# Kernel tuning notes

Measured on AMD Instinct MI355X. Metric: run time of the kernel, lower is better.

The kernel has to match this reference:

```python
import jax, jax.numpy as jnp
import numpy as np
from jax.scipy.special import logsumexp

B, S, K = 512, 2048, 17

def setup_inputs() -> dict:
    key = jax.random.key(0)
    k_em, k_lab, k_len, k_st, k_en, k_tr = jax.random.split(key, 6)
    emissions = jax.random.normal(k_em, (B, S, K), dtype=jnp.float32)
    labels = jax.random.randint(k_lab, (B, S), 0, K, dtype=jnp.int64).astype(jnp.int32)
    # ragged valid-prefix mask; torchcrf requires mask[:, 0] to be all True
    lengths = jax.random.randint(k_len, (B,), 1, S + 1)
    attention_mask = (jnp.arange(S)[None, :] < lengths[:, None]).astype(jnp.int32)
    # CRF params (torchcrf inits uniform(-0.1, 0.1))
    start_transitions = jax.random.uniform(k_st, (K,), minval=-0.1, maxval=0.1, dtype=jnp.float32)
    end_transitions = jax.random.uniform(k_en, (K,), minval=-0.1, maxval=0.1, dtype=jnp.float32)
    transitions = jax.random.uniform(k_tr, (K, K), minval=-0.1, maxval=0.1, dtype=jnp.float32)
    return {
        "emissions": emissions,
        "start_transitions": start_transitions,
        "end_transitions": end_transitions,
        "transitions": transitions,
        "labels": labels,
        "attention_mask": attention_mask,
    }


def _crf_neg_log_likelihood(emissions, start_transitions, end_transitions, transitions,
                            labels, mask_bool):
    # emissions: [B,S,K], labels: [B,S] int, mask_bool: [B,S] bool (mask[:,0] all True)
    mask_f = mask_bool.astype(emissions.dtype)
    b_idx = jnp.arange(emissions.shape[0])

    # ---- numerator: score of the gold path ----
    first_tags = labels[:, 0]                                  # [B]
    num = start_transitions[first_tags] + emissions[b_idx, 0, first_tags]
    prev_tags = labels[:, :-1]                                 # [B,S-1]
    cur_tags = labels[:, 1:]                                   # [B,S-1]
    emit_t = jnp.take_along_axis(emissions[:, 1:, :], cur_tags[..., None], axis=-1)[..., 0]
    step_scores = transitions[prev_tags, cur_tags] + emit_t    # [B,S-1]
    num = num + jnp.sum(step_scores * mask_f[:, 1:], axis=1)
    seq_ends = jnp.sum(mask_bool, axis=1).astype(jnp.int32) - 1  # [B]
    last_tags = jnp.take_along_axis(labels, seq_ends[:, None], axis=1)[:, 0]
    num = num + end_transitions[last_tags]

    # ---- denominator: log partition via forward algorithm (lax.scan over time) ----
    alpha0 = start_transitions[None, :] + emissions[:, 0, :]   # [B,K]

    def step(alpha, xs):
        emit, m = xs                                           # emit [B,K], m [B] bool
        # alpha[b, i] + transitions[i, j] + emit[b, j] -> logsumexp over i
        nxt = logsumexp(alpha[:, :, None] + transitions[None, :, :] + emit[:, None, :], axis=1)
        alpha = jnp.where(m[:, None], nxt, alpha)
        return alpha, None

    em_seq = jnp.swapaxes(emissions[:, 1:, :], 0, 1)           # [S-1,B,K]
    m_seq = jnp.swapaxes(mask_bool[:, 1:], 0, 1)               # [S-1,B]
    alpha, _ = jax.lax.scan(step, alpha0, (em_seq, m_seq))
    log_z = logsumexp(alpha + end_transitions[None, :], axis=1)  # [B]

    llh = num - log_z
    return -jnp.mean(llh)  # torchcrf reduction='mean', loss = -crf(...)


def reference(emissions, start_transitions, end_transitions, transitions, labels, attention_mask):
    mask_bool = attention_mask.astype(bool) & (labels >= 0)
    labels_c = jnp.where(labels == -100, 0, labels)
    loss = _crf_neg_log_likelihood(emissions, start_transitions, end_transitions,
                                   transitions, labels_c, mask_bool)
    return loss, emissions
```

## Files before the change

### kernel.cpp

```cpp
#include <hip/hip_runtime.h>
#include <cstddef>

#define NB 512
#define NS 2048
#define NK 17
#define CL 8
#define NW 4
#define HT 1024
#define SP 8
#define NLT (HT + SP)
#define CHUNKD 37
#define ROWD 9
#define LDS_DW ((NLT / 4) * CHUNKD)
#define SLABF (HT * NK)

typedef __fp16 h2 __attribute__((ext_vector_type(2)));
typedef float  f4 __attribute__((ext_vector_type(4)));
union UH { unsigned int u; h2 h; };

__global__ void prep_k(const float* __restrict__ trans, const int* __restrict__ attn,
                       unsigned int* __restrict__ Mg, int* __restrict__ lens) {
    __shared__ int red[4];
    const int tid = threadIdx.x;
    if (blockIdx.x == 0) {
        if (tid < 9 * NK) {
            int kk = tid / NK, n = tid % NK;
            float lo = __expf(trans[(2 * kk) * NK + n]);
            float hi = (kk < 8) ? __expf(trans[(2 * kk + 1) * NK + n]) : 0.f;
            UH u; u.h = __builtin_amdgcn_cvt_pkrtz(lo, hi);
            Mg[tid] = u.u;
        }
        return;
    }
    const int b = blockIdx.x - 1;
    const int4* __restrict__ a4 = (const int4*)(attn + (size_t)b * NS);
    int4 x = a4[tid];
    int4 y = a4[tid + 256];
    int s = x.x + x.y + x.z + x.w + y.x + y.y + y.z + y.w;
#pragma unroll
    for (int off = 32; off >= 1; off >>= 1) s += __shfl_down(s, off, 64);
    if ((tid & 63) == 0) red[tid >> 6] = s;
    __syncthreads();
    if (tid == 0) lens[b] = red[0] + red[1] + red[2] + red[3];
}

__global__ __launch_bounds__(256, 4) void crf_fused(
    const float* __restrict__ emis,
    const float* __restrict__ startT,
    const float* __restrict__ endT,
    const float* __restrict__ trans,
    const int*   __restrict__ labels,
    const int*   __restrict__ lens,
    const unsigned int* __restrict__ Mg,
    float*       __restrict__ outE,
    float*       __restrict__ out)
{
    __shared__ unsigned int expE[LDS_DW];
    float* red = (float*)expE;

    const int tid = threadIdx.x;

    if (blockIdx.x >= NB * 2) {
        const size_t off = (size_t)(blockIdx.x - NB * 2) * SLABF;
        const float* __restrict__ src = emis + off;
        float*       __restrict__ dst = outE + off;
        const int base = tid * 4;
        f4 r0 = *(const f4*)(src + base);
        f4 r1 = *(const f4*)(src + base + 1024);
        f4 r2 = *(const f4*)(src + base + 2048);
        f4 r3 = *(const f4*)(src + base + 3072);
#pragma unroll
        for (int k = 0; k < 3; ++k) {
            const int o = k * 4096 + base;
            f4 n0 = *(const f4*)(src + o + 4096);
            f4 n1 = *(const f4*)(src + o + 5120);
            f4 n2 = *(const f4*)(src + o + 6144);
            f4 n3 = *(const f4*)(src + o + 7168);
            __builtin_nontemporal_store(r0, (f4*)(dst + o));
            __builtin_nontemporal_store(r1, (f4*)(dst + o + 1024));
            __builtin_nontemporal_store(r2, (f4*)(dst + o + 2048));
            __builtin_nontemporal_store(r3, (f4*)(dst + o + 3072));
            r0 = n0; r1 = n1; r2 = n2; r3 = n3;
        }
        const int o = 12288 + base;
        f4 n0 = *(const f4*)(src + o + 4096);
        __builtin_nontemporal_store(r0, (f4*)(dst + o));
        __builtin_nontemporal_store(r1, (f4*)(dst + o + 1024));
        __builtin_nontemporal_store(r2, (f4*)(dst + o + 2048));
        __builtin_nontemporal_store(r3, (f4*)(dst + o + 3072));
        __builtin_nontemporal_store(n0, (f4*)(dst + o + 4096));
        return;
    }

    const int b  = blockIdx.x >> 1;
    const int h  = blockIdx.x & 1;
    const int T0 = h << 10;
    const int len = lens[b];

    if (T0 >= len) return;

    const size_t ebOff = (size_t)b * NS * NK;
    const float* __restrict__ eb = emis + ebOff;
    const int*   __restrict__ lb = labels + (size_t)b * NS;

    {
        const int startF = ((h == 0) ? 0 : (T0 - SP)) * NK;
        const int Tstop  = (len < T0 + HT) ? len : (T0 + HT);
        const int stopF  = Tstop * NK;
        int g = startF + tid * 4;
        int t4  = (int)((unsigned)g / 17u);
        int n4  = g - t4 * 17;
        int lt4 = t4 - (T0 - SP);
        f4 v = {0.f, 0.f, 0.f, 0.f};
        if (g < stopF) v = *(const f4*)(eb + g);
        while (g < stopF) {
            const int gn = g + 1024;
            f4 vn = v;
            if (gn < stopF) vn = *(const f4*)(eb + gn);
            float ev[4] = {v.x, v.y, v.z, v.w};
            int lt = lt4, nn = n4;
#pragma unroll
            for (int u = 0; u < 4; ++u) {
                if (g + u < stopF) {
                    int ha = ((lt >> 2) * CHUNKD + (lt & 3) * ROWD) * 2 + nn;
                    ((__fp16*)expE)[ha] = (__fp16)__expf(ev[u]);
                }
                ++nn; if (nn == 17) { nn = 0; ++lt; }
            }
            lt4 += 60; n4 += 4; if (n4 >= 17) { n4 -= 17; ++lt4; }
            v = vn; g = gn;
        }
    }
    __syncthreads();

    float numA = 0.f, zc = 0.f;

    if (tid >= 128) {
        int t = T0 + (tid - 128);
#pragma unroll
        for (int j = 0; j < 8; ++j, t += 128) {
            if (t < len) {
                int la = lb[t];
                numA += eb[(size_t)t * NK + la];
                numA += (t == 0) ? startT[la] : trans[lb[t - 1] * NK + la];
                if (t == len - 1) numA += endT[la];
            }
        }
    } else if (T0 + ((tid & 64) << 3) < len) {
        const int gc = h * 128 + tid;
        const int t0 = gc * CL;
        const int cE = (len - 1) >> 3;
        float logscale = 0.f, endlog = 0.f;
        bool hasEnd = false;
        h2 wh[9];
        {
            const __fp16 iv = (__fp16)(1.f / NK);
#pragma unroll
            for (int kk = 0; kk < 9; ++kk) { wh[kk].x = iv; wh[kk].y = iv; }
            wh[8].y = (__fp16)0.f;
        }

        if (gc == 0) {
            float wf[NK]; float ssum = 0.f;
            const int bdw = (SP >> 2) * CHUNKD;
#pragma unroll
            for (int k = 0; k < 9; ++k) {
                UH u; u.u = expE[bdw + k];
                int n = 2 * k;
                wf[n] = __expf(startT[n]) * (float)u.h.x;
                if (n + 1 < NK) wf[n + 1] = __expf(startT[n + 1]) * (float)u.h.y;
            }
#pragma unroll
            for (int n = 0; n < NK; ++n) ssum += wf[n];
            float r = 1.f / ssum;
            logscale = __logf(ssum);
#pragma unroll
            for (int kk = 0; kk < 8; ++kk)
                wh[kk] = __builtin_amdgcn_cvt_pkrtz(wf[2 * kk] * r, wf[2 * kk + 1] * r);
            wh[8] = __builtin_amdgcn_cvt_pkrtz(wf[16] * r, 0.f);
            if (len == 1) {
                float sd = 0.f;
#pragma unroll
                for (int n = 0; n < NK; ++n) sd += wf[n] * __expf(endT[n]);
                endlog = __logf(sd);
                hasEnd = true;
            }
        }

#pragma unroll 1
        for (int i = 0; i < CL + NW; ++i) {
            int t = t0 - NW + i;
            bool active = (t >= 1);
            int ta = active ? t : 1;
            int lt = ta - (T0 - SP);
            int bdw = (lt >> 2) * CHUNKD + (lt & 3) * ROWD;
            float ex[NK + 1];
#pragma unroll
            for (int k = 0; k < 9; ++k) {
                UH u; u.u = expE[bdw + k];
                ex[2 * k]     = (float)u.h.x;
                ex[2 * k + 1] = (float)u.h.y;
            }
            if (gc != 0 && t == t0) logscale = 0.f;

            float acc[NK];
#pragma unroll
            for (int n = 0; n < NK; ++n) acc[n] = 0.f;
#pragma unroll
            for (int kk = 0; kk < 9; ++kk) {
                h2 w = wh[kk];
#pragma unroll
                for (int n = 0; n < NK; ++n) {
                    UH u; u.u = Mg[kk * NK + n];
                    acc[n] = __builtin_amdgcn_fdot2(w, u.h, acc[n], false);
                }
            }
            float wf[NK]; float ssum = 0.f;
#pragma unroll
            for (int n = 0; n < NK; ++n) {
                float w = acc[n] * ex[n];
                wf[n] = w;
                ssum += w;
            }
            float r  = __builtin_amdgcn_rcpf(ssum);
            float lg = __logf(ssum);
            if (active) {
                if (t >= t0 && t == len - 1) {
                    float sd = 0.f;
#pragma unroll
                    for (int n = 0; n < NK; ++n) sd += wf[n] * __expf(endT[n]);
                    endlog = logscale + __logf(sd);
                    hasEnd = true;
                }
                logscale += lg;
#pragma unroll
                for (int kk = 0; kk < 8; ++kk)
                    wh[kk] = __builtin_amdgcn_cvt_pkrtz(wf[2 * kk] * r, wf[2 * kk + 1] * r);
                wh[8] = __builtin_amdgcn_cvt_pkrtz(wf[16] * r, 0.f);
            }
        }

        zc = ((gc < cE) ? logscale : 0.f) + (hasEnd ? endlog : 0.f);
    }

    __syncthreads();
    red[tid] = numA - zc;
    __syncthreads();
    for (int k = 128; k >= 1; k >>= 1) { if (tid < k) red[tid] += red[tid + k]; __syncthreads(); }
    if (tid == 0) atomicAdd(out, -red[0] * (1.f / (float)NB));
}

extern "C" void kernel_launch(void* const* d_in, const int* in_sizes, int n_in,
                              void* d_out, int out_size, void* d_ws, size_t ws_size,
                              hipStream_t stream) {
    (void)in_sizes; (void)n_in; (void)out_size; (void)ws_size;
    const float* emis   = (const float*)d_in[0];
    const float* startT = (const float*)d_in[1];
    const float* endT   = (const float*)d_in[2];
    const float* trans  = (const float*)d_in[3];
    const int*   labels = (const int*)d_in[4];
    const int*   attn   = (const int*)d_in[5];
    float* out = (float*)d_out;
    unsigned int* Mg = (unsigned int*)d_ws;
    int* lens        = (int*)((char*)d_ws + 1024);

    (void)hipMemsetAsync(d_out, 0, sizeof(float), stream);
    prep_k<<<NB + 1, 256, 0, stream>>>(trans, attn, Mg, lens);
    crf_fused<<<NB * 4, 256, 0, stream>>>(emis, startT, endT, trans, labels,
                                          lens, Mg, out + 1, out);
}
```

Before: 156.6 us.

## Drop LDS exp staging; read emissions directly per chunk with prefetch

Removes the shared-memory fp16 exp(emission) staging pass and the two-halves-per-batch split. Each batch is now handled by one block whose 256 threads each run one 8-step chunk, reading emission rows from global memory with a one-row prefetch and computing exp inline. Numerator work is now done by the same threads, using vectorized label loads. Copy blocks are interleaved with compute blocks (two copies per batch). This removes an LDS barrier and the LDS footprint, which should raise occupancy, at the cost of strided global loads that are not coalesced and of redundant exp evaluations in the warm-up steps.

```diff
diff --git a/kernel.cpp b/kernel.cpp
--- a/kernel.cpp
+++ b/kernel.cpp
@@ -6,13 +6,7 @@
 #define NK 17
 #define CL 8
 #define NW 4
-#define HT 1024
-#define SP 8
-#define NLT (HT + SP)
-#define CHUNKD 37
-#define ROWD 9
-#define LDS_DW ((NLT / 4) * CHUNKD)
-#define SLABF (HT * NK)
+#define SLABF (1024 * NK)
 
 typedef __fp16 h2 __attribute__((ext_vector_type(2)));
 typedef float  f4 __attribute__((ext_vector_type(4)));
@@ -44,6 +38,35 @@
     if (tid == 0) lens[b] = red[0] + red[1] + red[2] + red[3];
 }
 
+__device__ __forceinline__ void copy_slab(const float* __restrict__ src,
+                                          float* __restrict__ dst, int tid) {
+    const int base = tid * 4;
+    f4 r0 = *(const f4*)(src + base);
+    f4 r1 = *(const f4*)(src + base + 1024);
+    f4 r2 = *(const f4*)(src + base + 2048);
+    f4 r3 = *(const f4*)(src + base + 3072);
+#pragma unroll
+    for (int k = 0; k < 3; ++k) {
+        const int o = k * 4096 + base;
+        f4 n0 = *(const f4*)(src + o + 4096);
+        f4 n1 = *(const f4*)(src + o + 5120);
+        f4 n2 = *(const f4*)(src + o + 6144);
+        f4 n3 = *(const f4*)(src + o + 7168);
+        __builtin_nontemporal_store(r0, (f4*)(dst + o));
+        __builtin_nontemporal_store(r1, (f4*)(dst + o + 1024));
+        __builtin_nontemporal_store(r2, (f4*)(dst + o + 2048));
+        __builtin_nontemporal_store(r3, (f4*)(dst + o + 3072));
+        r0 = n0; r1 = n1; r2 = n2; r3 = n3;
+    }
+    const int o = 12288 + base;
+    f4 n0 = *(const f4*)(src + o + 4096);
+    __builtin_nontemporal_store(r0, (f4*)(dst + o));
+    __builtin_nontemporal_store(r1, (f4*)(dst + o + 1024));
+    __builtin_nontemporal_store(r2, (f4*)(dst + o + 2048));
+    __builtin_nontemporal_store(r3, (f4*)(dst + o + 3072));
+    __builtin_nontemporal_store(n0, (f4*)(dst + o + 4096));
+}
+
 __global__ __launch_bounds__(256, 4) void crf_fused(
     const float* __restrict__ emis,
     const float* __restrict__ startT,
@@ -55,100 +78,46 @@
     float*       __restrict__ outE,
     float*       __restrict__ out)
 {
-    __shared__ unsigned int expE[LDS_DW];
-    float* red = (float*)expE;
-
+    __shared__ float red[256];
     const int tid = threadIdx.x;
-
-    if (blockIdx.x >= NB * 2) {
-        const size_t off = (size_t)(blockIdx.x - NB * 2) * SLABF;
-        const float* __restrict__ src = emis + off;
-        float*       __restrict__ dst = outE + off;
-        const int base = tid * 4;
-        f4 r0 = *(const f4*)(src + base);
-        f4 r1 = *(const f4*)(src + base + 1024);
-        f4 r2 = *(const f4*)(src + base + 2048);
-        f4 r3 = *(const f4*)(src + base + 3072);
-#pragma unroll
-        for (int k = 0; k < 3; ++k) {
-            const int o = k * 4096 + base;
-            f4 n0 = *(const f4*)(src + o + 4096);
-            f4 n1 = *(const f4*)(src + o + 5120);
-            f4 n2 = *(const f4*)(src + o + 6144);
-            f4 n3 = *(const f4*)(src + o + 7168);
-            __builtin_nontemporal_store(r0, (f4*)(dst + o));
-            __builtin_nontemporal_store(r1, (f4*)(dst + o + 1024));
-            __builtin_nontemporal_store(r2, (f4*)(dst + o + 2048));
-            __builtin_nontemporal_store(r3, (f4*)(dst + o + 3072));
-            r0 = n0; r1 = n1; r2 = n2; r3 = n3;
-        }
-        const int o = 12288 + base;
-        f4 n0 = *(const f4*)(src + o + 4096);
-        __builtin_nontemporal_store(r0, (f4*)(dst + o));
-        __builtin_nontemporal_store(r1, (f4*)(dst + o + 1024));
-        __builtin_nontemporal_store(r2, (f4*)(dst + o + 2048));
-        __builtin_nontemporal_store(r3, (f4*)(dst + o + 3072));
-        __builtin_nontemporal_store(n0, (f4*)(dst + o + 4096));
+    const int rb  = blockIdx.x / 3;
+    const int rk  = blockIdx.x - rb * 3;
+
+    if (rk != 0) {
+        const size_t off = ((size_t)rb * 2 + (rk - 1)) * SLABF;
+        copy_slab(emis + off, outE + off, tid);
         return;
     }
 
-    const int b  = blockIdx.x >> 1;
-    const int h  = blockIdx.x & 1;
-    const int T0 = h << 10;
+    const int b   = rb;
     const int len = lens[b];
-
-    if (T0 >= len) return;
-
     const size_t ebOff = (size_t)b * NS * NK;
     const float* __restrict__ eb = emis + ebOff;
     const int*   __restrict__ lb = labels + (size_t)b * NS;
 
-    {
-        const int startF = ((h == 0) ? 0 : (T0 - SP)) * NK;
-        const int Tstop  = (len < T0 + HT) ? len : (T0 + HT);
-        const int stopF  = Tstop * NK;
-        int g = startF + tid * 4;
-        int t4  = (int)((unsigned)g / 17u);
-        int n4  = g - t4 * 17;
-        int lt4 = t4 - (T0 - SP);
-        f4 v = {0.f, 0.f, 0.f, 0.f};
-        if (g < stopF) v = *(const f4*)(eb + g);
-        while (g < stopF) {
-            const int gn = g + 1024;
-            f4 vn = v;
-            if (gn < stopF) vn = *(const f4*)(eb + gn);
-            float ev[4] = {v.x, v.y, v.z, v.w};
-            int lt = lt4, nn = n4;
-#pragma unroll
-            for (int u = 0; u < 4; ++u) {
-                if (g + u < stopF) {
-                    int ha = ((lt >> 2) * CHUNKD + (lt & 3) * ROWD) * 2 + nn;
-                    ((__fp16*)expE)[ha] = (__fp16)__expf(ev[u]);
+    float numA = 0.f, zc = 0.f;
+    const int gc = tid;
+    const int t0 = gc * CL;
+
+    if (((tid >> 6) << 9) < len) {
+        if (t0 < len) {
+            int4 La = *(const int4*)(lb + t0);
+            int4 Lc = *(const int4*)(lb + t0 + 4);
+            int lab[8] = {La.x, La.y, La.z, La.w, Lc.x, Lc.y, Lc.z, Lc.w};
+            int lp = (gc > 0) ? lb[t0 - 1] : 0;
+#pragma unroll
+            for (int j = 0; j < 8; ++j) {
+                int t = t0 + j;
+                if (t < len) {
+                    int la = lab[j];
+                    numA += eb[(size_t)t * NK + la];
+                    numA += (t == 0) ? startT[la]
+                                     : trans[((j == 0) ? lp : lab[j - 1]) * NK + la];
+                    if (t == len - 1) numA += endT[la];
                 }
-                ++nn; if (nn == 17) { nn = 0; ++lt; }
-            }
-            lt4 += 60; n4 += 4; if (n4 >= 17) { n4 -= 17; ++lt4; }
-            v = vn; g = gn;
-        }
-    }
-    __syncthreads();
-
-    float numA = 0.f, zc = 0.f;
-
-    if (tid >= 128) {
-        int t = T0 + (tid - 128);
-#pragma unroll
-        for (int j = 0; j < 8; ++j, t += 128) {
-            if (t < len) {
-                int la = lb[t];
-                numA += eb[(size_t)t * NK + la];
-                numA += (t == 0) ? startT[la] : trans[lb[t - 1] * NK + la];
-                if (t == len - 1) numA += endT[la];
-            }
-        }
-    } else if (T0 + ((tid & 64) << 3) < len) {
-        const int gc = h * 128 + tid;
-        const int t0 = gc * CL;
+            }
+        }
+
         const int cE = (len - 1) >> 3;
         float logscale = 0.f, endlog = 0.f;
         bool hasEnd = false;
@@ -162,16 +131,11 @@
 
         if (gc == 0) {
             float wf[NK]; float ssum = 0.f;
-            const int bdw = (SP >> 2) * CHUNKD;
-#pragma unroll
-            for (int k = 0; k < 9; ++k) {
-                UH u; u.u = expE[bdw + k];
-                int n = 2 * k;
-                wf[n] = __expf(startT[n]) * (float)u.h.x;
-                if (n + 1 < NK) wf[n + 1] = __expf(startT[n + 1]) * (float)u.h.y;
-            }
-#pragma unroll
-            for (int n = 0; n < NK; ++n) ssum += wf[n];
+#pragma unroll
+            for (int n = 0; n < NK; ++n) {
+                wf[n] = __expf(startT[n]) * __expf(eb[n]);
+                ssum += wf[n];
+            }
             float r = 1.f / ssum;
             logscale = __logf(ssum);
 #pragma unroll
@@ -187,20 +151,27 @@
             }
         }
 
+        int tP = t0 - NW; if (tP < 1) tP = 1;
+        const float* rp = eb + (size_t)tP * NK;
+        f4 A0 = *(const f4*)rp, B0 = *(const f4*)(rp + 4);
+        f4 C0 = *(const f4*)(rp + 8), D0 = *(const f4*)(rp + 12);
+        float E0 = rp[16];
+
 #pragma unroll 1
         for (int i = 0; i < CL + NW; ++i) {
             int t = t0 - NW + i;
             bool active = (t >= 1);
-            int ta = active ? t : 1;
-            int lt = ta - (T0 - SP);
-            int bdw = (lt >> 2) * CHUNKD + (lt & 3) * ROWD;
-            float ex[NK + 1];
-#pragma unroll
-            for (int k = 0; k < 9; ++k) {
-                UH u; u.u = expE[bdw + k];
-                ex[2 * k]     = (float)u.h.x;
-                ex[2 * k + 1] = (float)u.h.y;
-            }
+            int tn = t + 1;
+            if (tn < 1) tn = 1;
+            if (tn > NS - 1) tn = NS - 1;
+            const float* rpn = eb + (size_t)tn * NK;
+            f4 A1 = *(const f4*)rpn, B1 = *(const f4*)(rpn + 4);
+            f4 C1 = *(const f4*)(rpn + 8), D1 = *(const f4*)(rpn + 12);
+            float E1 = rpn[16];
+
+            float r[NK] = {A0.x, A0.y, A0.z, A0.w, B0.x, B0.y, B0.z, B0.w,
+                           C0.x, C0.y, C0.z, C0.w, D0.x, D0.y, D0.z, D0.w, E0};
+
             if (gc != 0 && t == t0) logscale = 0.f;
 
             float acc[NK];
@@ -218,11 +189,11 @@
             float wf[NK]; float ssum = 0.f;
 #pragma unroll
             for (int n = 0; n < NK; ++n) {
-                float w = acc[n] * ex[n];
+                float w = acc[n] * __expf(r[n]);
                 wf[n] = w;
                 ssum += w;
             }
-            float r  = __builtin_amdgcn_rcpf(ssum);
+            float rr = __builtin_amdgcn_rcpf(ssum);
             float lg = __logf(ssum);
             if (active) {
                 if (t >= t0 && t == len - 1) {
@@ -235,15 +206,15 @@
                 logscale += lg;
 #pragma unroll
                 for (int kk = 0; kk < 8; ++kk)
-                    wh[kk] = __builtin_amdgcn_cvt_pkrtz(wf[2 * kk] * r, wf[2 * kk + 1] * r);
-                wh[8] = __builtin_amdgcn_cvt_pkrtz(wf[16] * r, 0.f);
-            }
+                    wh[kk] = __builtin_amdgcn_cvt_pkrtz(wf[2 * kk] * rr, wf[2 * kk + 1] * rr);
+                wh[8] = __builtin_amdgcn_cvt_pkrtz(wf[16] * rr, 0.f);
+            }
+            A0 = A1; B0 = B1; C0 = C1; D0 = D1; E0 = E1;
         }
 
         zc = ((gc < cE) ? logscale : 0.f) + (hasEnd ? endlog : 0.f);
     }
 
-    __syncthreads();
     red[tid] = numA - zc;
     __syncthreads();
     for (int k = 128; k >= 1; k >>= 1) { if (tid < k) red[tid] += red[tid + k]; __syncthreads(); }
@@ -266,6 +237,6 @@
 
     (void)hipMemsetAsync(d_out, 0, sizeof(float), stream);
     prep_k<<<NB + 1, 256, 0, stream>>>(trans, attn, Mg, lens);
-    crf_fused<<<NB * 4, 256, 0, stream>>>(emis, startT, endT, trans, labels,
+    crf_fused<<<NB * 3, 256, 0, stream>>>(emis, startT, endT, trans, labels,
                                           lens, Mg, out + 1, out);
 }
```

Result: slower. 168.0 us (+7.3%).
